# Kernel optimization log

Measured on AMD Instinct MI355X. Metric: run time of the kernel, lower is better.

The kernel has to match this reference:

```python
import jax, jax.numpy as jnp
import numpy as np

EPS = 1e-5
N_CAMERAS, N_POINTS = 6, 4


def _bilinear_sample(feats, gx, gy):
    # feats: [B, C, H, W]; gx, gy: [B, Q] in [-1, 1]; align_corners=False, zero padding
    B, C, H, W = feats.shape
    ix = ((gx + 1.0) * W - 1.0) * 0.5
    iy = ((gy + 1.0) * H - 1.0) * 0.5
    x0 = jnp.floor(ix)
    y0 = jnp.floor(iy)
    fx = ix - x0
    fy = iy - y0
    x0i = x0.astype(jnp.int32)
    y0i = y0.astype(jnp.int32)
    ff = feats.reshape(B, C, H * W)

    def corner(xi, yi, w):
        valid = (xi >= 0) & (xi < W) & (yi >= 0) & (yi < H)
        idx = jnp.clip(yi, 0, H - 1) * W + jnp.clip(xi, 0, W - 1)
        v = jnp.take_along_axis(ff, idx[:, None, :], axis=2)  # [B, C, Q]
        return v * (w * valid)[:, None, :]

    return (corner(x0i, y0i, (1 - fx) * (1 - fy))
            + corner(x0i + 1, y0i, fx * (1 - fy))
            + corner(x0i, y0i + 1, (1 - fx) * fy)
            + corner(x0i + 1, y0i + 1, fx * fy))


def setup_inputs() -> dict:
    key = jax.random.key(0)
    ks = jax.random.split(key, 8)
    Hb = Wb = 128
    nq = Hb * Wb
    bs, hidden, N, P = 2, 256, N_CAMERAS, N_POINTS
    C, Hf, Wf = 256, 28, 50

    rho = jnp.broadcast_to((jnp.arange(Hb, dtype=jnp.float32) / Hb)[:, None], (Hb, Wb))
    phi = jnp.broadcast_to((jnp.arange(Wb, dtype=jnp.float32) / Wb)[None, :], (Hb, Wb))
    pc_range = jnp.array([51.2, 2.0 * np.pi, -5.0, 3.0], jnp.float32)
    intervals = jnp.array([51.2 / Hb, 2.0 * np.pi / Wb], jnp.float32)
    img_size = jnp.array([1600.0, 900.0], jnp.float32)

    # realistic pinhole lidar->image matrices for 6 surround cameras
    K = np.array([[1200.0, 0, 800, 0], [0, 1200.0, 450, 0], [0, 0, 1, 0], [0, 0, 0, 1]], np.float32)
    mats = []
    for i in range(N):
        yaw = 2.0 * np.pi * i / N
        c, s = np.cos(yaw), np.sin(yaw)
        R = np.array([[s, -c, 0], [0, 0, -1], [c, s, 0]], np.float32)  # x_right, y_down, z_forward
        E = np.eye(4, dtype=np.float32)
        E[:3, :3] = R
        E[:3, 3] = np.array([0.0, 1.5, 0.5], np.float32)
        mats.append(K @ E)
    lidar2imgs = jnp.asarray(np.broadcast_to(np.stack(mats), (bs, N, 4, 4)).copy())

    return {
        'query': jax.random.normal(ks[0], (nq, bs, hidden), jnp.float32),
        'query_pos': jax.random.normal(ks[1], (nq, bs, hidden), jnp.float32),
        'rho': rho,
        'phi': phi,
        'zz_cord': jax.random.uniform(ks[2], (bs, nq, 1), jnp.float32),
        'img_feats': jax.random.normal(ks[3], (bs, N, C, Hf, Wf), jnp.float32),
        'lidar2imgs': lidar2imgs,
        'intervals': intervals,
        'pc_range': pc_range,
        'img_size': img_size,
        'Wa': jax.random.normal(ks[4], (hidden, N * P), jnp.float32) * 0.02,
        'ba': jnp.zeros((N * P,), jnp.float32),
        'Wo': jax.random.normal(ks[5], (hidden, hidden), jnp.float32) * 0.02,
        'bo': jnp.zeros((hidden,), jnp.float32),
    }


def reference(query, query_pos, rho, phi, zz_cord, img_feats, lidar2imgs,
              intervals, pc_range, img_size, Wa, ba, Wo, bo):
    q = jnp.transpose(query + query_pos, (1, 0, 2))  # [bs, nq, h]
    bs, nq, _ = q.shape
    aw = (q @ Wa + ba).reshape(bs, 1, nq, N_CAMERAS, N_POINTS)

    # polar BEV -> cartesian lidar coords
    r = rho.reshape(-1, 1) * pc_range[0] + intervals[0] / 2  # [nq, 1]
    p = phi.reshape(-1, 1) * pc_range[1] - jnp.pi + intervals[1] / 2
    xx = r * jnp.cos(p)
    yy = r * jnp.sin(p)
    zz = zz_cord * (pc_range[3] - pc_range[2]) + pc_range[2]  # [bs, nq, 1]
    xyz = jnp.concatenate([
        jnp.broadcast_to(xx[None], (bs, nq, 1)),
        jnp.broadcast_to(yy[None], (bs, nq, 1)),
        zz,
        jnp.ones((bs, nq, 1), q.dtype),
    ], axis=-1)  # [bs, nq, 4]

    cam = jnp.einsum('bnij,bqj->bnqi', lidar2imgs, xyz)  # [bs, N, nq, 4]
    zc = cam[..., 2]
    gx = cam[..., 0] / jnp.maximum(zc, EPS) / img_size[0]
    gy = cam[..., 1] / jnp.maximum(zc, EPS) / img_size[1]
    gx = (gx - 0.5) * 2.0
    gy = (gy - 0.5) * 2.0
    mask = (zc > EPS) & (gx > -1.0) & (gx < 1.0) & (gy > -1.0) & (gy < 1.0)  # [bs, N, nq]

    B, N, C, H, W = img_feats.shape
    sampled = _bilinear_sample(img_feats.reshape(B * N, C, H, W),
                               gx.reshape(B * N, nq), gy.reshape(B * N, nq))
    sampled = jnp.nan_to_num(sampled.reshape(B, N, C, nq).transpose(0, 2, 3, 1))  # [bs, C, nq, N]

    maskf = mask.transpose(0, 2, 1)[:, None, :, :, None].astype(q.dtype)  # [bs,1,nq,N,1]
    ws = (jax.nn.sigmoid(aw) * maskf).sum(-1)  # [bs, 1, nq, N]
    out = jnp.einsum('bcqn,bqn->bcq', sampled, ws[:, 0])  # [bs, C, nq]
    out = out.transpose(2, 0, 1) @ Wo + bo + query  # dropout p=0 -> identity
    mask_out = mask.transpose(0, 2, 1)[:, None, :, :, None]  # [bs,1,nq,N,1] bool
    return out, mask_out
```

## Files before the change

### kernel.cpp

```cpp
#include <hip/hip_runtime.h>
#include <hip/hip_bf16.h>
#include <math.h>

#define NQ    16384
#define BS    2
#define HID   256
#define NCAM  6
#define NPTS  4
#define CF    256
#define HF    28
#define WF    50
#define HWF   (HF*WF)
#define NIMG  (BS*NCAM)
#define EPSV  1e-5f

typedef __attribute__((ext_vector_type(8))) short short8v;
typedef __attribute__((ext_vector_type(4))) float float4v;

__device__ __forceinline__ unsigned short f2bf(float f) {
    unsigned u = __float_as_uint(f);
    u += 0x7fffu + ((u >> 16) & 1u);
    return (unsigned short)(u >> 16);
}
__device__ __forceinline__ unsigned pkbf(float lo, float hi) {
    __hip_bfloat162 h = __float22bfloat162_rn(float2{lo, hi});
    return *reinterpret_cast<unsigned*>(&h);
}
__device__ __forceinline__ float bfLO(unsigned u) { return __uint_as_float(u << 16); }
__device__ __forceinline__ float bfHI(unsigned u) { return __uint_as_float(u & 0xffff0000u); }

__global__ __launch_bounds__(256) void prep_aw(
    const float* __restrict__ feats, const float* __restrict__ Wo,
    const float* __restrict__ Wa,    const float* __restrict__ query,
    const float* __restrict__ query_pos, const float* __restrict__ ba,
    const float* __restrict__ rho,   const float* __restrict__ phi,
    const float* __restrict__ zz,    const float* __restrict__ l2i,
    const float* __restrict__ intervals, const float* __restrict__ pc_range,
    const float* __restrict__ img_size,
    unsigned short* __restrict__ featsT, unsigned short* __restrict__ WoT,
    float* __restrict__ ws, float* __restrict__ gxy, float* __restrict__ out)
{
    __shared__ __align__(16) char smem[32 * 264 * 2];

    const int tx = threadIdx.x & 31;
    const int ty = threadIdx.x >> 5;
    if (blockIdx.x < 528) {
        float (*tile)[33] = reinterpret_cast<float(*)[33]>(smem);
        const int img = blockIdx.x / 44;
        const int hw0 = (blockIdx.x % 44) * 32;
        for (int ct = 0; ct < 8; ++ct) {
            const int c0 = ct * 32;
            #pragma unroll
            for (int i = 0; i < 4; ++i) {
                const int c  = c0 + ty + 8 * i;
                const int hw = hw0 + tx;
                tile[ty + 8 * i][tx] = (hw < HWF) ? feats[((size_t)img * CF + c) * HWF + hw] : 0.f;
            }
            __syncthreads();
            #pragma unroll
            for (int i = 0; i < 4; ++i) {
                const int hw = hw0 + ty + 8 * i;
                if (hw < HWF)
                    featsT[((size_t)img * HWF + hw) * CF + c0 + tx] = f2bf(tile[tx][ty + 8 * i]);
            }
            __syncthreads();
        }
    } else if (blockIdx.x < 592) {
        float (*tile)[33] = reinterpret_cast<float(*)[33]>(smem);
        const int bid = blockIdx.x - 528;
        const int kt = bid >> 3, nt = bid & 7;
        #pragma unroll
        for (int i = 0; i < 4; ++i)
            tile[ty + 8 * i][tx] = Wo[(size_t)(kt * 32 + ty + 8 * i) * HID + nt * 32 + tx];
        __syncthreads();
        #pragma unroll
        for (int i = 0; i < 4; ++i)
            WoT[(size_t)(nt * 32 + ty + 8 * i) * HID + kt * 32 + tx] = f2bf(tile[tx][ty + 8 * i]);
    } else if (blockIdx.x < 1104) {
        unsigned short (*waL)[264] = reinterpret_cast<unsigned short(*)[264]>(smem);
        #pragma unroll
        for (int s = 0; s < 32; ++s)
            waL[s][threadIdx.x] = (s < 24) ? f2bf(Wa[threadIdx.x * 24 + s]) : (unsigned short)0;
        __syncthreads();

        const int bid  = blockIdx.x - 592;
        const int wave = threadIdx.x >> 6;
        const int lane = threadIdx.x & 63;
        const int arow = lane & 15;
        const int g4   = lane >> 4;
        const int g0   = (bid * 4 + wave) * 16;
        const int ga   = g0 + arow;
        const int bb   = ga >> 14;
        const int qq   = ga & (NQ - 1);
        const float* qp1 = query     + ((size_t)qq * BS + bb) * HID;
        const float* qp2 = query_pos + ((size_t)qq * BS + bb) * HID;

        float4v aw0 = {0.f,0.f,0.f,0.f}, aw1 = {0.f,0.f,0.f,0.f};
        #pragma unroll
        for (int kk = 0; kk < 8; ++kk) {
            const int k0 = kk * 32 + g4 * 8;
            const float4 a0 = *reinterpret_cast<const float4*>(qp1 + k0);
            const float4 a1 = *reinterpret_cast<const float4*>(qp1 + k0 + 4);
            const float4 p0 = *reinterpret_cast<const float4*>(qp2 + k0);
            const float4 p1 = *reinterpret_cast<const float4*>(qp2 + k0 + 4);
            union { uint4 u; short8v s; } af;
            af.u.x = pkbf(a0.x + p0.x, a0.y + p0.y);
            af.u.y = pkbf(a0.z + p0.z, a0.w + p0.w);
            af.u.z = pkbf(a1.x + p1.x, a1.y + p1.y);
            af.u.w = pkbf(a1.z + p1.z, a1.w + p1.w);
            const short8v b0 = *reinterpret_cast<const short8v*>(&waL[arow][k0]);
            const short8v b1 = *reinterpret_cast<const short8v*>(&waL[16 + arow][k0]);
            aw0 = __builtin_amdgcn_mfma_f32_16x16x32_bf16(af.s, b0, aw0, 0, 0, 0);
            aw1 = __builtin_amdgcn_mfma_f32_16x16x32_bf16(af.s, b1, aw1, 0, 0, 0);
        }
        const float ba0 = ba[arow];
        const float ba1 = (arow < 8) ? ba[16 + arow] : 0.f;
        #pragma unroll
        for (int i = 0; i < 4; ++i) {
            float s0 = 1.0f / (1.0f + __expf(-(aw0[i] + ba0)));
            float s1 = (arow < 8) ? 1.0f / (1.0f + __expf(-(aw1[i] + ba1))) : 0.f;
            s0 += __shfl_xor(s0, 1);  s0 += __shfl_xor(s0, 2);
            s1 += __shfl_xor(s1, 1);  s1 += __shfl_xor(s1, 2);
            if ((arow & 3) == 0) {
                const int gq = g0 + g4 * 4 + i;
                ws[(size_t)gq * 8 + (arow >> 2)] = s0;
                if (arow < 8)
                    ws[(size_t)gq * 8 + 4 + (arow >> 2)] = s1;
            }
        }
    } else {
        const int pair = (blockIdx.x - 1104) * 256 + threadIdx.x;
        const int gq   = pair / 6;
        const int cam  = pair - gq * 6;
        const int bb   = gq >> 14;
        const int qn   = gq & (NQ - 1);
        const float pc0 = pc_range[0], pc1 = pc_range[1];
        const float pc2 = pc_range[2], pc3 = pc_range[3];
        const float rr = rho[qn] * pc0 + intervals[0] * 0.5f;
        const float pp = phi[qn] * pc1 - 3.14159265358979323846f + intervals[1] * 0.5f;
        const float xx = rr * cosf(pp);
        const float yy = rr * sinf(pp);
        const float z  = zz[bb * NQ + qn] * (pc3 - pc2) + pc2;
        const float* M = l2i + (bb * NCAM + cam) * 16;
        const float cx = M[0]*xx + M[1]*yy + M[2]*z  + M[3];
        const float cy = M[4]*xx + M[5]*yy + M[6]*z  + M[7];
        const float cz = M[8]*xx + M[9]*yy + M[10]*z + M[11];
        const float d  = fmaxf(cz, EPSV);
        const float gx = (cx / d / img_size[0] - 0.5f) * 2.0f;
        const float gy = (cy / d / img_size[1] - 0.5f) * 2.0f;
        const bool  mk = (cz > EPSV) && (gx > -1.0f) && (gx < 1.0f)
                                     && (gy > -1.0f) && (gy < 1.0f);
        gxy[(size_t)gq * 12 + cam * 2]     = mk ? gx : -3.0f;
        gxy[(size_t)gq * 12 + cam * 2 + 1] = mk ? gy : 0.0f;
        out[(size_t)NQ * BS * HID + pair]  = mk ? 1.0f : 0.0f;
    }
}

__global__ __launch_bounds__(512) void ca_main12(
    const float* __restrict__ query, const unsigned short* __restrict__ featsT,
    const float* __restrict__ ws,    const float* __restrict__ gxy,
    const unsigned short* __restrict__ WoT, const float* __restrict__ bo,
    float* __restrict__ out)
{
    __shared__ char fab[16 * 512];

    const int tid  = threadIdx.x;
    const int wave = tid >> 6;
    const int lane = tid & 63;
    const int l32  = lane & 31;
    const int r    = wave * 2 + (lane >> 5);
    const int base = blockIdx.x * 16;
    const int b    = base >> 14;
    const int g    = base + r;

    const float wsn = ws[(size_t)g * 8 + (l32 & 7)];
    const float gv  = (l32 < 12) ? gxy[(size_t)g * 12 + l32] : 0.f;

    float gxs[NCAM], gys[NCAM], wsv[NCAM];
    bool  msk[NCAM];
    #pragma unroll
    for (int n = 0; n < NCAM; ++n) {
        gxs[n] = __shfl(gv, (lane & 32) + 2 * n);
        gys[n] = __shfl(gv, (lane & 32) + 2 * n + 1);
        msk[n] = gxs[n] > -2.0f;
        wsv[n] = msk[n] ? __shfl(wsn, (lane & 32) + n) : 0.f;
    }

    float acc[8] = {0.f,0.f,0.f,0.f,0.f,0.f,0.f,0.f};
    for (int n = 0; n < NCAM; ++n) {
        if (msk[n]) {
            const float ixf = ((gxs[n] + 1.0f) * WF - 1.0f) * 0.5f;
            const float iyf = ((gys[n] + 1.0f) * HF - 1.0f) * 0.5f;
            const float x0f = floorf(ixf), y0f = floorf(iyf);
            const float fx = ixf - x0f, fy = iyf - y0f;
            const int x0 = (int)x0f, y0 = (int)y0f;
            const int   xs[4] = {x0, x0 + 1, x0,     x0 + 1};
            const int   ys[4] = {y0, y0,     y0 + 1, y0 + 1};
            const float wc[4] = {(1.f-fx)*(1.f-fy), fx*(1.f-fy),
                                 (1.f-fx)*fy,       fx*fy};
            const unsigned short* fb = featsT + (size_t)(b * NCAM + n) * HWF * CF + 8 * l32;
            #pragma unroll
            for (int c4 = 0; c4 < 4; ++c4) {
                const bool v = (xs[c4] >= 0) && (xs[c4] < WF) &&
                               (ys[c4] >= 0) && (ys[c4] < HF);
                const int xc = min(max(xs[c4], 0), WF - 1);
                const int yc = min(max(ys[c4], 0), HF - 1);
                const float wnv = wsv[n] * (v ? wc[c4] : 0.0f);
                const uint4 u = *reinterpret_cast<const uint4*>(fb + (size_t)(yc * WF + xc) * CF);
                acc[0] += wnv * bfLO(u.x); acc[1] += wnv * bfHI(u.x);
                acc[2] += wnv * bfLO(u.y); acc[3] += wnv * bfHI(u.y);
                acc[4] += wnv * bfLO(u.z); acc[5] += wnv * bfHI(u.z);
                acc[6] += wnv * bfLO(u.w); acc[7] += wnv * bfHI(u.w);
            }
        }
    }

    {
        uint4 u;
        u.x = pkbf(acc[0], acc[1]);
        u.y = pkbf(acc[2], acc[3]);
        u.z = pkbf(acc[4], acc[5]);
        u.w = pkbf(acc[6], acc[7]);
        *reinterpret_cast<uint4*>(fab + ((unsigned)(r * 512 + 16 * l32) ^ ((unsigned)(r & 7) << 4))) = u;
    }
    __syncthreads();

    const int colw = lane & 15;
    const int g4   = lane >> 4;
    #pragma unroll
    for (int t = 0; t < 2; ++t) {
        const int col = wave * 16 + t * 128 + colw;
        float4v dacc = {0.f,0.f,0.f,0.f};
        #pragma unroll
        for (int kk = 0; kk < 8; ++kk) {
            const int k0 = kk * 32 + g4 * 8;
            const short8v af = *reinterpret_cast<const short8v*>(
                fab + ((unsigned)(colw * 512 + k0 * 2) ^ ((unsigned)(colw & 7) << 4)));
            const short8v bw = *reinterpret_cast<const short8v*>(
                WoT + (size_t)col * HID + k0);
            dacc = __builtin_amdgcn_mfma_f32_16x16x32_bf16(af, bw, dacc, 0, 0, 0);
        }
        #pragma unroll
        for (int rg = 0; rg < 4; ++rg) {
            const int row = g4 * 4 + rg;
            const int gq = base + row;
            const int bq = gq >> 14, qq = gq & (NQ - 1);
            const size_t addr = ((size_t)qq * BS + bq) * HID + col;
            out[addr] = dacc[rg] + bo[col] + query[addr];
        }
    }
}

__global__ __launch_bounds__(256) void prep_all(
    const float* __restrict__ feats, const float* __restrict__ Wo,
    const float* __restrict__ Wa, unsigned short* __restrict__ featsT,
    unsigned short* __restrict__ WoT, unsigned short* __restrict__ WaT)
{
    __shared__ float tile[32][33];
    const int tx = threadIdx.x & 31;
    const int ty = threadIdx.x >> 5;
    if (blockIdx.x < 528) {
        const int img = blockIdx.x / 44;
        const int hw0 = (blockIdx.x % 44) * 32;
        for (int ct = 0; ct < 8; ++ct) {
            const int c0 = ct * 32;
            #pragma unroll
            for (int i = 0; i < 4; ++i) {
                const int c  = c0 + ty + 8 * i;
                const int hw = hw0 + tx;
                tile[ty + 8 * i][tx] = (hw < HWF) ? feats[((size_t)img * CF + c) * HWF + hw] : 0.f;
            }
            __syncthreads();
            #pragma unroll
            for (int i = 0; i < 4; ++i) {
                const int hw = hw0 + ty + 8 * i;
                if (hw < HWF)
                    featsT[((size_t)img * HWF + hw) * CF + c0 + tx] = f2bf(tile[tx][ty + 8 * i]);
            }
            __syncthreads();
        }
    } else if (blockIdx.x < 592) {
        const int bid = blockIdx.x - 528;
        const int kt = bid >> 3, nt = bid & 7;
        #pragma unroll
        for (int i = 0; i < 4; ++i)
            tile[ty + 8 * i][tx] = Wo[(size_t)(kt * 32 + ty + 8 * i) * HID + nt * 32 + tx];
        __syncthreads();
        #pragma unroll
        for (int i = 0; i < 4; ++i)
            WoT[(size_t)(nt * 32 + ty + 8 * i) * HID + kt * 32 + tx] = f2bf(tile[tx][ty + 8 * i]);
    } else {
        const int bid = blockIdx.x - 592;
        #pragma unroll
        for (int v = 0; v < 4; ++v) {
            const int idx = bid * 1024 + v * 256 + threadIdx.x;
            const int j = idx >> 8, k = idx & 255;
            WaT[idx] = (j < 24) ? f2bf(Wa[k * 24 + j]) : (unsigned short)0;
        }
    }
}

__global__ __launch_bounds__(512) void ca_fused3(
    const float* __restrict__ query, const float* __restrict__ query_pos,
    const float* __restrict__ rho,   const float* __restrict__ phi,
    const float* __restrict__ zz,    const unsigned short* __restrict__ featsT,
    const float* __restrict__ l2i,   const float* __restrict__ intervals,
    const float* __restrict__ pc_range, const float* __restrict__ img_size,
    const unsigned short* __restrict__ WaT, const float* __restrict__ ba,
    const unsigned short* __restrict__ WoT, const float* __restrict__ bo,
    float* __restrict__ out)
{
    __shared__ char  fab[16 * 512];
    __shared__ float awl[16][36];
    const int tid  = threadIdx.x;
    const int wave = tid >> 6;
    const int lane = tid & 63;
    const int l32  = lane & 31;
    const int r    = wave * 2 + (lane >> 5);
    const int base = blockIdx.x * 16;
    const int g    = base + r;
    const int b    = g >> 14;
    const int q    = g & (NQ - 1);
    const size_t qrow = ((size_t)q * BS + b) * HID;
    {
        const float4 a0 = *reinterpret_cast<const float4*>(&query[qrow + 8 * l32]);
        const float4 a1 = *reinterpret_cast<const float4*>(&query[qrow + 8 * l32 + 4]);
        const float4 p0 = *reinterpret_cast<const float4*>(&query_pos[qrow + 8 * l32]);
        const float4 p1 = *reinterpret_cast<const float4*>(&query_pos[qrow + 8 * l32 + 4]);
        uint4 u;
        u.x = ((unsigned)f2bf(a0.y + p0.y) << 16) | f2bf(a0.x + p0.x);
        u.y = ((unsigned)f2bf(a0.w + p0.w) << 16) | f2bf(a0.z + p0.z);
        u.z = ((unsigned)f2bf(a1.y + p1.y) << 16) | f2bf(a1.x + p1.x);
        u.w = ((unsigned)f2bf(a1.w + p1.w) << 16) | f2bf(a1.z + p1.z);
        *reinterpret_cast<uint4*>(fab + ((unsigned)(r * 512 + 16 * l32) ^ ((unsigned)(r & 7) << 4))) = u;
    }
    float gxs[NCAM], gys[NCAM];
    bool  msk[NCAM];
    {
        const float pc0 = pc_range[0], pc1 = pc_range[1];
        const float pc2 = pc_range[2], pc3 = pc_range[3];
        const float rr = rho[q] * pc0 + intervals[0] * 0.5f;
        const float pp = phi[q] * pc1 - 3.14159265358979323846f + intervals[1] * 0.5f;
        const float xx = rr * cosf(pp);
        const float yy = rr * sinf(pp);
        const float z  = zz[b * NQ + q] * (pc3 - pc2) + pc2;
        const float iw = img_size[0], ih = img_size[1];
        #pragma unroll
        for (int n = 0; n < NCAM; ++n) {
            const float* M = l2i + (b * NCAM + n) * 16;
            const float cx = M[0]*xx + M[1]*yy + M[2]*z  + M[3];
            const float cy = M[4]*xx + M[5]*yy + M[6]*z  + M[7];
            const float cz = M[8]*xx + M[9]*yy + M[10]*z + M[11];
            const float d  = fmaxf(cz, EPSV);
            const float gx = (cx / d / iw - 0.5f) * 2.0f;
            const float gy = (cy / d / ih - 0.5f) * 2.0f;
            msk[n] = (cz > EPSV) && (gx > -1.0f) && (gx < 1.0f)
                                 && (gy > -1.0f) && (gy < 1.0f);
            gxs[n] = gx; gys[n] = gy;
        }
    }
    if (l32 < NCAM)
        out[(size_t)NQ * BS * HID + ((size_t)b * NQ + q) * NCAM + l32] =
            msk[l32] ? 1.0f : 0.0f;
    __syncthreads();
    if (wave < 2) {
        const int arow = lane & 15;
        const int g4   = lane >> 4;
        float4v aw = {0.f,0.f,0.f,0.f};
        #pragma unroll
        for (int kk = 0; kk < 8; ++kk) {
            const int k0 = kk * 32 + g4 * 8;
            const short8v af = *reinterpret_cast<const short8v*>(
                fab + ((unsigned)(arow * 512 + k0 * 2) ^ ((unsigned)(arow & 7) << 4)));
            const short8v bw = *reinterpret_cast<const short8v*>(
                WaT + (size_t)(wave * 16 + arow) * HID + k0);
            aw = __builtin_amdgcn_mfma_f32_16x16x32_bf16(af, bw, aw, 0, 0, 0);
        }
        #pragma unroll
        for (int i = 0; i < 4; ++i)
            awl[g4 * 4 + i][wave * 16 + arow] = aw[i];
    }
    __syncthreads();
    float wsv[NCAM];
    {
        float sv = 0.f;
        if (l32 < 24) {
            const float x = awl[r][l32] + ba[l32];
            sv = 1.0f / (1.0f + __expf(-x));
        }
        sv += __shfl_xor(sv, 1);
        sv += __shfl_xor(sv, 2);
        #pragma unroll
        for (int n = 0; n < NCAM; ++n)
            wsv[n] = __shfl(sv, (lane & 32) + 4 * n);
    }
    float acc[8] = {0.f,0.f,0.f,0.f,0.f,0.f,0.f,0.f};
    for (int n = 0; n < NCAM; ++n) {
        if (msk[n]) {
            const float ixf = ((gxs[n] + 1.0f) * WF - 1.0f) * 0.5f;
            const float iyf = ((gys[n] + 1.0f) * HF - 1.0f) * 0.5f;
            const float x0f = floorf(ixf), y0f = floorf(iyf);
            const float fx = ixf - x0f, fy = iyf - y0f;
            const int x0 = (int)x0f, y0 = (int)y0f;
            const int   xs[4] = {x0, x0 + 1, x0,     x0 + 1};
            const int   ys[4] = {y0, y0,     y0 + 1, y0 + 1};
            const float wc[4] = {(1.f-fx)*(1.f-fy), fx*(1.f-fy),
                                 (1.f-fx)*fy,       fx*fy};
            const unsigned short* fb = featsT + (size_t)(b * NCAM + n) * HWF * CF + 8 * l32;
            #pragma unroll
            for (int c4 = 0; c4 < 4; ++c4) {
                const bool v = (xs[c4] >= 0) && (xs[c4] < WF) &&
                               (ys[c4] >= 0) && (ys[c4] < HF);
                const int xc = min(max(xs[c4], 0), WF - 1);
                const int yc = min(max(ys[c4], 0), HF - 1);
                const float wnv = wsv[n] * (v ? wc[c4] : 0.0f);
                const uint4 u = *reinterpret_cast<const uint4*>(fb + (size_t)(yc * WF + xc) * CF);
                acc[0] += wnv * bfLO(u.x); acc[1] += wnv * bfHI(u.x);
                acc[2] += wnv * bfLO(u.y); acc[3] += wnv * bfHI(u.y);
                acc[4] += wnv * bfLO(u.z); acc[5] += wnv * bfHI(u.z);
                acc[6] += wnv * bfLO(u.w); acc[7] += wnv * bfHI(u.w);
            }
        }
    }
    {
        uint4 u;
        u.x = ((unsigned)f2bf(acc[1]) << 16) | f2bf(acc[0]);
        u.y = ((unsigned)f2bf(acc[3]) << 16) | f2bf(acc[2]);
        u.z = ((unsigned)f2bf(acc[5]) << 16) | f2bf(acc[4]);
        u.w = ((unsigned)f2bf(acc[7]) << 16) | f2bf(acc[6]);
        *reinterpret_cast<uint4*>(fab + ((unsigned)(r * 512 + 16 * l32) ^ ((unsigned)(r & 7) << 4))) = u;
    }
    __syncthreads();
    const int colw = lane & 15;
    const int g4   = lane >> 4;
    #pragma unroll
    for (int t = 0; t < 2; ++t) {
        const int col = wave * 16 + t * 128 + colw;
        float4v dacc = {0.f,0.f,0.f,0.f};
        #pragma unroll
        for (int kk = 0; kk < 8; ++kk) {
            const int k0 = kk * 32 + g4 * 8;
            const short8v af = *reinterpret_cast<const short8v*>(
                fab + ((unsigned)(colw * 512 + k0 * 2) ^ ((unsigned)(colw & 7) << 4)));
            const short8v bw = *reinterpret_cast<const short8v*>(
                WoT + (size_t)col * HID + k0);
            dacc = __builtin_amdgcn_mfma_f32_16x16x32_bf16(af, bw, dacc, 0, 0, 0);
        }
        #pragma unroll
        for (int rg = 0; rg < 4; ++rg) {
            const int row = g4 * 4 + rg;
            const int gq = base + row;
            const int bq = gq >> 14, qq = gq & (NQ - 1);
            const size_t addr = ((size_t)qq * BS + bq) * HID + col;
            out[addr] = dacc[rg] + bo[col] + query[addr];
        }
    }
}

#define CHUNK 32
__global__ __launch_bounds__(512, 2) void ca_fused_fb(
    const float* __restrict__ query, const float* __restrict__ query_pos,
    const float* __restrict__ rho, const float* __restrict__ phi,
    const float* __restrict__ zz, const float* __restrict__ feats,
    const float* __restrict__ l2i, const float* __restrict__ intervals,
    const float* __restrict__ pc_range, const float* __restrict__ img_size,
    const float* __restrict__ Wa, const float* __restrict__ ba,
    const float* __restrict__ Wo, const float* __restrict__ bo,
    float* __restrict__ out)
{
    __shared__ float fa[8][HID];
    __shared__ float wolds[CHUNK][HID];
    const int tid  = threadIdx.x;
    const int wave = tid >> 6;
    const int lane = tid & 63;
    const int g    = blockIdx.x * 8 + wave;
    const int b    = g / NQ;
    const int q    = g - b * NQ;
    const size_t qrow = ((size_t)q * BS + b) * HID;
    {
        float qv[4];
        #pragma unroll
        for (int k = 0; k < 4; ++k) {
            const int h = lane + 64 * k;
            qv[k] = query[qrow + h] + query_pos[qrow + h];
        }
        const float pc0 = pc_range[0], pc1 = pc_range[1];
        const float pc2 = pc_range[2], pc3 = pc_range[3];
        const float r = rho[q] * pc0 + intervals[0] * 0.5f;
        const float p = phi[q] * pc1 - 3.14159265358979323846f + intervals[1] * 0.5f;
        const float xx = r * cosf(p);
        const float yy = r * sinf(p);
        const float z  = zz[b * NQ + q] * (pc3 - pc2) + pc2;
        const float iw = img_size[0], ih = img_size[1];
        float gxs[NCAM], gys[NCAM], wss[NCAM];
        bool  msk[NCAM];
        #pragma unroll
        for (int n = 0; n < NCAM; ++n) {
            const float* M = l2i + (b * NCAM + n) * 16;
            const float cx = M[0]*xx + M[1]*yy + M[2]*z  + M[3];
            const float cy = M[4]*xx + M[5]*yy + M[6]*z  + M[7];
            const float cz = M[8]*xx + M[9]*yy + M[10]*z + M[11];
            const float d  = fmaxf(cz, EPSV);
            const float gx = (cx / d / iw - 0.5f) * 2.0f;
            const float gy = (cy / d / ih - 0.5f) * 2.0f;
            msk[n] = (cz > EPSV) && (gx > -1.0f) && (gx < 1.0f)
                                 && (gy > -1.0f) && (gy < 1.0f);
            gxs[n] = gx; gys[n] = gy; wss[n] = 0.0f;
        }
        for (int n = 0; n < NCAM; ++n) {
            if (!msk[n]) continue;
            float s = 0.0f;
            #pragma unroll
            for (int pp = 0; pp < NPTS; ++pp) {
                const int j = n * NPTS + pp;
                float part = 0.0f;
                #pragma unroll
                for (int k = 0; k < 4; ++k)
                    part += qv[k] * Wa[(lane + 64 * k) * 24 + j];
                #pragma unroll
                for (int off = 32; off; off >>= 1)
                    part += __shfl_xor(part, off, 64);
                s += 1.0f / (1.0f + expf(-(part + ba[j])));
            }
            wss[n] = s;
        }
        if (lane < NCAM)
            out[(size_t)NQ * BS * HID + ((size_t)b * NQ + q) * NCAM + lane] =
                msk[lane] ? 1.0f : 0.0f;
        float acc[4] = {0.f,0.f,0.f,0.f};
        for (int n = 0; n < NCAM; ++n) {
            if (!msk[n]) continue;
            const float ixf = ((gxs[n] + 1.0f) * WF - 1.0f) * 0.5f;
            const float iyf = ((gys[n] + 1.0f) * HF - 1.0f) * 0.5f;
            const float x0f = floorf(ixf), y0f = floorf(iyf);
            const float fx = ixf - x0f, fy = iyf - y0f;
            const int x0 = (int)x0f, y0 = (int)y0f;
            const int   xs[4] = {x0, x0 + 1, x0,     x0 + 1};
            const int   ys[4] = {y0, y0,     y0 + 1, y0 + 1};
            const float wc[4] = {(1.f-fx)*(1.f-fy), fx*(1.f-fy),
                                 (1.f-fx)*fy,       fx*fy};
            int   offc[4];
            float wv[4];
            #pragma unroll
            for (int c4 = 0; c4 < 4; ++c4) {
                const bool v = (xs[c4] >= 0) && (xs[c4] < WF) &&
                               (ys[c4] >= 0) && (ys[c4] < HF);
                const int xc = min(max(xs[c4], 0), WF - 1);
                const int yc = min(max(ys[c4], 0), HF - 1);
                offc[c4] = yc * WF + xc;
                wv[c4]   = v ? wc[c4] : 0.0f;
            }
            const float wn = wss[n];
            const float* fbp = feats + (size_t)(b * NCAM + n) * CF * HWF;
            #pragma unroll
            for (int k = 0; k < 4; ++k) {
                const float* fc = fbp + (size_t)(lane + 64 * k) * HWF;
                const float sv = wv[0]*fc[offc[0]] + wv[1]*fc[offc[1]]
                               + wv[2]*fc[offc[2]] + wv[3]*fc[offc[3]];
                acc[k] += wn * sv;
            }
        }
        #pragma unroll
        for (int k = 0; k < 4; ++k)
            fa[wave][lane + 64 * k] = acc[k];
    }
    float racc[4] = {0.f,0.f,0.f,0.f};
    const int h0 = 4 * lane;
    for (int c0 = 0; c0 < HID; c0 += CHUNK) {
        __syncthreads();
        for (int i = tid; i < CHUNK * HID; i += 512)
            wolds[i >> 8][i & 255] = Wo[(size_t)(c0 + (i >> 8)) * HID + (i & 255)];
        __syncthreads();
        #pragma unroll 8
        for (int c = 0; c < CHUNK; ++c) {
            const float fav = fa[wave][c0 + c];
            const float4 wv4 = *reinterpret_cast<const float4*>(&wolds[c][h0]);
            racc[0] += fav * wv4.x;
            racc[1] += fav * wv4.y;
            racc[2] += fav * wv4.z;
            racc[3] += fav * wv4.w;
        }
    }
    float4 o;
    o.x = racc[0] + bo[h0 + 0] + query[qrow + h0 + 0];
    o.y = racc[1] + bo[h0 + 1] + query[qrow + h0 + 1];
    o.z = racc[2] + bo[h0 + 2] + query[qrow + h0 + 2];
    o.w = racc[3] + bo[h0 + 3] + query[qrow + h0 + 3];
    *reinterpret_cast<float4*>(&out[qrow + h0]) = o;
}

extern "C" void kernel_launch(void* const* d_in, const int* in_sizes, int n_in,
                              void* d_out, int out_size, void* d_ws, size_t ws_size,
                              hipStream_t stream) {
    const float* query     = (const float*)d_in[0];
    const float* query_pos = (const float*)d_in[1];
    const float* rho       = (const float*)d_in[2];
    const float* phi       = (const float*)d_in[3];
    const float* zz        = (const float*)d_in[4];
    const float* feats     = (const float*)d_in[5];
    const float* l2i       = (const float*)d_in[6];
    const float* intervals = (const float*)d_in[7];
    const float* pc_range  = (const float*)d_in[8];
    const float* img_size  = (const float*)d_in[9];
    const float* Wa        = (const float*)d_in[10];
    const float* ba        = (const float*)d_in[11];
    const float* Wo        = (const float*)d_in[12];
    const float* bo        = (const float*)d_in[13];
    float* out = (float*)d_out;

    const size_t featsT_bytes = (size_t)NIMG * HWF * CF * 2;
    const size_t woT_bytes    = (size_t)HID * HID * 2;
    const size_t waT_bytes    = (size_t)32 * HID * 2;
    const size_t ws_bytes     = (size_t)BS * NQ * 8 * 4;
    const size_t gxy_bytes    = (size_t)BS * NQ * 12 * 4;
    const size_t need_small   = featsT_bytes + woT_bytes + waT_bytes;
    const size_t need_full    = featsT_bytes + woT_bytes + ws_bytes + gxy_bytes;

    if (ws_size >= need_full) {
        unsigned short* featsT = (unsigned short*)d_ws;
        unsigned short* WoT    = (unsigned short*)((char*)d_ws + featsT_bytes);
        float*          wsb    = (float*)((char*)d_ws + featsT_bytes + woT_bytes);
        float*          gxy    = (float*)((char*)d_ws + featsT_bytes + woT_bytes + ws_bytes);
        prep_aw<<<1872, 256, 0, stream>>>(feats, Wo, Wa, query, query_pos, ba,
                                          rho, phi, zz, l2i, intervals, pc_range,
                                          img_size, featsT, WoT, wsb, gxy, out);
        ca_main12<<<2048, 512, 0, stream>>>(query, featsT, wsb, gxy, WoT, bo, out);
    } else if (ws_size >= need_small) {
        unsigned short* featsT = (unsigned short*)d_ws;
        unsigned short* WoT    = (unsigned short*)((char*)d_ws + featsT_bytes);
        unsigned short* WaT    = (unsigned short*)((char*)d_ws + featsT_bytes + woT_bytes);
        prep_all<<<600, 256, 0, stream>>>(feats, Wo, Wa, featsT, WoT, WaT);
        ca_fused3<<<2048, 512, 0, stream>>>(query, query_pos, rho, phi, zz,
                                            featsT, l2i, intervals, pc_range,
                                            img_size, WaT, ba, WoT, bo, out);
    } else {
        ca_fused_fb<<<(BS * NQ) / 8, 512, 0, stream>>>(query, query_pos, rho, phi, zz,
                                                       feats, l2i, intervals, pc_range,
                                                       img_size, Wa, ba, Wo, bo, out);
    }
}
```

Measured before the change: 67.01 us.

## Batch gather and weight loads via inline asm, interleave batch blocks

The bilinear gather now issues all four corner loads with inline asm and waits once, instead of load-then-accumulate per corner. The output projection likewise issues all eight Wo loads plus the LDS reads before a single wait and the MFMA chain. Block IDs are remapped so consecutive blocks alternate between the two batch halves, and launch_bounds gains an occupancy hint. The aim is more memory-level parallelism and a more even spread of work across the batch halves. In exchange, the hand-placed waits and sched barriers limit what the compiler can schedule, and the extra live registers may lower occupancy.

```diff
diff --git a/kernel.cpp b/kernel.cpp
--- a/kernel.cpp
+++ b/kernel.cpp
@@ -156,7 +156,7 @@
     }
 }
 
-__global__ __launch_bounds__(512) void ca_main12(
+__global__ __launch_bounds__(512, 4) void ca_main14(
     const float* __restrict__ query, const unsigned short* __restrict__ featsT,
     const float* __restrict__ ws,    const float* __restrict__ gxy,
     const unsigned short* __restrict__ WoT, const float* __restrict__ bo,
@@ -169,8 +169,12 @@
     const int lane = tid & 63;
     const int l32  = lane & 31;
     const int r    = wave * 2 + (lane >> 5);
-    const int base = blockIdx.x * 16;
-    const int b    = base >> 14;
+
+    const int bid  = blockIdx.x;
+    const int xg   = (bid & 7) >> 2;
+    const int idx  = (bid & 3) + ((bid >> 3) << 2);
+    const int base = (xg << 14) + idx * 16;
+    const int b    = xg;
     const int g    = base + r;
 
     const float wsn = ws[(size_t)g * 8 + (l32 & 7)];
@@ -199,18 +203,27 @@
             const float wc[4] = {(1.f-fx)*(1.f-fy), fx*(1.f-fy),
                                  (1.f-fx)*fy,       fx*fy};
             const unsigned short* fb = featsT + (size_t)(b * NCAM + n) * HWF * CF + 8 * l32;
+            uint4 u[4];
+            float w[4];
             #pragma unroll
             for (int c4 = 0; c4 < 4; ++c4) {
                 const bool v = (xs[c4] >= 0) && (xs[c4] < WF) &&
                                (ys[c4] >= 0) && (ys[c4] < HF);
                 const int xc = min(max(xs[c4], 0), WF - 1);
                 const int yc = min(max(ys[c4], 0), HF - 1);
-                const float wnv = wsv[n] * (v ? wc[c4] : 0.0f);
-                const uint4 u = *reinterpret_cast<const uint4*>(fb + (size_t)(yc * WF + xc) * CF);
-                acc[0] += wnv * bfLO(u.x); acc[1] += wnv * bfHI(u.x);
-                acc[2] += wnv * bfLO(u.y); acc[3] += wnv * bfHI(u.y);
-                acc[4] += wnv * bfLO(u.z); acc[5] += wnv * bfHI(u.z);
-                acc[6] += wnv * bfLO(u.w); acc[7] += wnv * bfHI(u.w);
+                const unsigned short* ap = fb + (size_t)(yc * WF + xc) * CF;
+                asm volatile("global_load_dwordx4 %0, %1, off"
+                             : "=v"(u[c4]) : "v"(ap));
+                w[c4] = wsv[n] * (v ? wc[c4] : 0.0f);
+            }
+            asm volatile("s_waitcnt vmcnt(0)" ::: "memory");
+            __builtin_amdgcn_sched_barrier(0);
+            #pragma unroll
+            for (int c4 = 0; c4 < 4; ++c4) {
+                acc[0] += w[c4] * bfLO(u[c4].x); acc[1] += w[c4] * bfHI(u[c4].x);
+                acc[2] += w[c4] * bfLO(u[c4].y); acc[3] += w[c4] * bfHI(u[c4].y);
+                acc[4] += w[c4] * bfLO(u[c4].z); acc[5] += w[c4] * bfHI(u[c4].z);
+                acc[6] += w[c4] * bfLO(u[c4].w); acc[7] += w[c4] * bfHI(u[c4].w);
             }
         }
     }
@@ -227,26 +240,42 @@
 
     const int colw = lane & 15;
     const int g4   = lane >> 4;
+    float4v dacc[2];
     #pragma unroll
     for (int t = 0; t < 2; ++t) {
         const int col = wave * 16 + t * 128 + colw;
-        float4v dacc = {0.f,0.f,0.f,0.f};
+        const unsigned short* bp = WoT + (size_t)col * HID + g4 * 8;
+        uint4 bw[8];
+        #pragma unroll
+        for (int i = 0; i < 8; ++i)
+            asm volatile("global_load_dwordx4 %0, %1, off"
+                         : "=v"(bw[i]) : "v"(bp + (size_t)i * 32));
+        short8v af[8];
+        #pragma unroll
+        for (int kk = 0; kk < 8; ++kk)
+            af[kk] = *reinterpret_cast<const short8v*>(
+                fab + ((unsigned)(colw * 512 + (kk * 32 + g4 * 8) * 2) ^ ((unsigned)(colw & 7) << 4)));
+        asm volatile("s_waitcnt vmcnt(0)" ::: "memory");
+        __builtin_amdgcn_sched_barrier(0);
+        float4v d = {0.f,0.f,0.f,0.f};
         #pragma unroll
         for (int kk = 0; kk < 8; ++kk) {
-            const int k0 = kk * 32 + g4 * 8;
-            const short8v af = *reinterpret_cast<const short8v*>(
-                fab + ((unsigned)(colw * 512 + k0 * 2) ^ ((unsigned)(colw & 7) << 4)));
-            const short8v bw = *reinterpret_cast<const short8v*>(
-                WoT + (size_t)col * HID + k0);
-            dacc = __builtin_amdgcn_mfma_f32_16x16x32_bf16(af, bw, dacc, 0, 0, 0);
-        }
+            union { uint4 u; short8v s; } bu; bu.u = bw[kk];
+            d = __builtin_amdgcn_mfma_f32_16x16x32_bf16(af[kk], bu.s, d, 0, 0, 0);
+        }
+        dacc[t] = d;
+    }
+    #pragma unroll
+    for (int t = 0; t < 2; ++t) {
+        const int col = wave * 16 + t * 128 + colw;
+        const float boc = bo[col];
         #pragma unroll
         for (int rg = 0; rg < 4; ++rg) {
             const int row = g4 * 4 + rg;
             const int gq = base + row;
             const int bq = gq >> 14, qq = gq & (NQ - 1);
             const size_t addr = ((size_t)qq * BS + bq) * HID + col;
-            out[addr] = dacc[rg] + bo[col] + query[addr];
+            out[addr] = dacc[t][rg] + boc + query[addr];
         }
     }
 }
@@ -624,7 +653,7 @@
         prep_aw<<<1872, 256, 0, stream>>>(feats, Wo, Wa, query, query_pos, ba,
                                           rho, phi, zz, l2i, intervals, pc_range,
                                           img_size, featsT, WoT, wsb, gxy, out);
-        ca_main12<<<2048, 512, 0, stream>>>(query, featsT, wsb, gxy, WoT, bo, out);
+        ca_main14<<<2048, 512, 0, stream>>>(query, featsT, wsb, gxy, WoT, bo, out);
     } else if (ws_size >= need_small) {
         unsigned short* featsT = (unsigned short*)d_ws;
         unsigned short* WoT    = (unsigned short*)((char*)d_ws + featsT_bytes);
```

After: 65.62 us, median of 2. 2.1% less time.
